# Kernel optimization log

Measured on AMD Instinct MI355X. Metric: run time of the kernel, lower is better.

Reference implementation:

```python
import jax, jax.numpy as jnp
import numpy as np

H = 768
NH = 12
DH = H // NH  # 64
EPS = 1e-6


def _split_heads(x):
    # [B,S,H] -> [B,NH,S,DH]
    B, S, _ = x.shape
    return x.reshape(B, S, NH, DH).transpose(0, 2, 1, 3)


def setup_inputs() -> dict:
    key = jax.random.key(0)
    ks = jax.random.split(key, 16)
    B, S = 4, 1024
    sc = 0.02
    return {
        "hidden_states": jax.random.normal(ks[0], (B, S, H), jnp.float32),
        "time_embeddings": jax.random.normal(ks[1], (B, S, H), jnp.float32),
        "space_embeddings": jax.random.normal(ks[2], (B, S, H), jnp.float32),
        "attention_mask": jnp.zeros((B, 1, 1, S), jnp.float32),
        "Wq": jax.random.normal(ks[3], (H, H), jnp.float32) * sc,
        "bq": jnp.zeros((H,), jnp.float32),
        "Wk": jax.random.normal(ks[4], (H, H), jnp.float32) * sc,
        "bk": jnp.zeros((H,), jnp.float32),
        "Wv": jax.random.normal(ks[5], (H, H), jnp.float32) * sc,
        "bv": jnp.zeros((H,), jnp.float32),
        "Wt": jax.random.normal(ks[6], (H, H), jnp.float32) * sc,
        "bt": jnp.zeros((H,), jnp.float32),
        "Ws": jax.random.normal(ks[7], (H, H), jnp.float32) * sc,
        "bs": jnp.zeros((H,), jnp.float32),
    }


def reference(hidden_states, time_embeddings, space_embeddings, attention_mask,
              Wq, bq, Wk, bk, Wv, bv, Wt, bt, Ws, bs):
    q = _split_heads(hidden_states @ Wq.T + bq)   # [B,NH,S,DH]
    k = _split_heads(hidden_states @ Wk.T + bk)
    v = _split_heads(hidden_states @ Wv.T + bv)
    T = _split_heads(time_embeddings @ Wt.T + bt)
    Sp = _split_heads(space_embeddings @ Ws.T + bs)

    base = jnp.einsum("bhqd,bhkd->bhqk", q, k)
    T_norm = jnp.linalg.norm(T, axis=-1, keepdims=True)          # [B,NH,S,1]
    time_sim = jnp.einsum("bhqd,bhkd->bhqk", T, T) / (T_norm + EPS)
    S_norm = jnp.linalg.norm(Sp, axis=-1, keepdims=True)
    space_sim = jnp.einsum("bhqd,bhkd->bhqk", Sp, Sp) / (S_norm + EPS)

    scores = base * time_sim * space_sim / jnp.sqrt(jnp.float32(DH))
    scores = scores + attention_mask
    probs = jax.nn.softmax(scores, axis=-1)  # dropout is identity in eval
    ctx = jnp.einsum("bhqk,bhkd->bhqd", probs, v)
    B, _, S, _ = ctx.shape
    return ctx.transpose(0, 2, 1, 3).reshape(B, S, H)
```

## Files before the change

### kernel.cpp

```cpp
#include <hip/hip_runtime.h>

#define NHEADS 12
#define SEQ    1024
#define HDIM   768
#define DHEAD  64
#define BH_TOT 48
#define EPSN   1e-6f

typedef __attribute__((ext_vector_type(8))) short    bf8;
typedef __attribute__((ext_vector_type(4))) float    fx4;
typedef __attribute__((ext_vector_type(4))) _Float16 h4;

#define SZT 3145728u
#define WSZ 589824u

__device__ __forceinline__ float bf2f(unsigned short h) {
  union { unsigned int u; float f; } v; v.u = ((unsigned int)h) << 16; return v.f;
}
__device__ __forceinline__ unsigned short f2bf(float f) {
  union { float f; unsigned int u; } v; v.f = f;
  unsigned int u = v.u;
  return (unsigned short)((u + 0x7FFFu + ((u >> 16) & 1u)) >> 16);
}

typedef __attribute__((address_space(3))) unsigned int lds_u32;
typedef __attribute__((address_space(1))) const unsigned int glb_u32;
__device__ __forceinline__ void gld16(const unsigned short* g, unsigned short* l) {
  __builtin_amdgcn_global_load_lds((glb_u32*)g, (lds_u32*)l, 16, 0, 0);
}

__global__ void convert_kernel(const float* __restrict__ hs, const float* __restrict__ te,
                               const float* __restrict__ se,
                               const float* __restrict__ Wq, const float* __restrict__ Wk,
                               const float* __restrict__ Wv, const float* __restrict__ Wt,
                               const float* __restrict__ Ws2,
                               unsigned short* __restrict__ ws)
{
  const int z = blockIdx.y;
  const float* src;
  unsigned short* dst;
  int n;
  if (z < 3) {
    src = (z == 0) ? hs : (z == 1) ? te : se;
    dst = ws + (size_t)(5 + z) * SZT;
    n = 3145728;
  } else {
    src = (z == 3) ? Wq : (z == 4) ? Wk : (z == 5) ? Wv : (z == 6) ? Wt : Ws2;
    dst = ws + (size_t)8 * SZT + (size_t)(z - 3) * WSZ;
    n = 589824;
  }
  const int base = (blockIdx.x * 256 + threadIdx.x) * 8;
  if (base >= n) return;
  const fx4 a = *(const fx4*)(src + base);
  const fx4 b = *(const fx4*)(src + base + 4);
  bf8 o;
#pragma unroll
  for (int j = 0; j < 4; ++j) { o[j] = (short)f2bf(a[j]); o[4 + j] = (short)f2bf(b[j]); }
  *(bf8*)(dst + base) = o;
}

__global__ __launch_bounds__(256, 3)
void proj_kernel(unsigned short* __restrict__ ws,
                 const float* __restrict__ bq, const float* __restrict__ bk,
                 const float* __restrict__ bv, const float* __restrict__ bt,
                 const float* __restrict__ bs)
{
  __shared__ unsigned short Xs[2][4096];
  __shared__ unsigned short Ys[2][4096];

  const int z = blockIdx.z;
  const unsigned short* X = ws + (size_t)5 * SZT + (size_t)((z < 3) ? 0 : (z - 2)) * SZT;
  const unsigned short* W = ws + (size_t)8 * SZT + (size_t)z * WSZ;
  const float* bias = (z == 0) ? bq : (z == 1) ? bk : (z == 2) ? bv : (z == 3) ? bt : bs;
  unsigned short* out = ws + (size_t)((z < 2) ? z : (z == 2) ? 4 : (z == 3) ? 2 : 3) * SZT;

  const int tid   = threadIdx.x;
  const int lane  = tid & 63;
  const int wid   = tid >> 6;
  const int wm    = wid >> 1, wn = wid & 1;
  const int colid = lane & 15, quad = lane >> 4;
  const int m0 = blockIdx.y * 128, n0 = blockIdx.x * 128;

  auto stage = [&](int kt, int pb) {
#pragma unroll
    for (int i = 0; i < 2; ++i) {
      const int slot = i * 256 + tid;
      const int row = slot >> 2, ch = slot & 3;
      gld16(X + (m0 + row) * HDIM + kt + ch * 8, &Xs[pb][slot * 8]);
      gld16(W + (n0 + row) * HDIM + kt + ch * 8, &Ys[pb][slot * 8]);
    }
  };

  fx4 acc[4][4];
#pragma unroll
  for (int i = 0; i < 4; ++i)
#pragma unroll
    for (int j = 0; j < 4; ++j) acc[i][j] = (fx4){0.f, 0.f, 0.f, 0.f};

  stage(0, 0);
  __syncthreads();

  for (int it = 0; it < 24; ++it) {
    const int pb = it & 1;
    if (it + 1 < 24) stage((it + 1) * 32, pb ^ 1);

    bf8 af[4], bfr[4];
#pragma unroll
    for (int i = 0; i < 4; ++i)
      af[i] = *(const bf8*)&Xs[pb][(wm * 64 + i * 16 + colid) * 32 + quad * 8];
#pragma unroll
    for (int j = 0; j < 4; ++j)
      bfr[j] = *(const bf8*)&Ys[pb][(wn * 64 + j * 16 + colid) * 32 + quad * 8];
#pragma unroll
    for (int i = 0; i < 4; ++i)
#pragma unroll
      for (int j = 0; j < 4; ++j)
        acc[i][j] = __builtin_amdgcn_mfma_f32_16x16x32_bf16(af[i], bfr[j], acc[i][j], 0, 0, 0);
    __syncthreads();
  }

  if (z != 2) {
#pragma unroll
    for (int i = 0; i < 4; ++i) {
      const int r0 = m0 + wm * 64 + i * 16 + quad * 4;
      const int bb = r0 >> 10, s0 = r0 & 1023;
#pragma unroll
      for (int j = 0; j < 4; ++j) {
        const int c = n0 + wn * 64 + j * 16 + colid;
        const int h = c >> 6, d = c & 63;
        const float bvl = bias[c];
        unsigned short* op = out + (((bb * NHEADS + h) * SEQ + s0) * DHEAD + d);
#pragma unroll
        for (int reg = 0; reg < 4; ++reg)
          op[reg * DHEAD] = f2bf(acc[i][j][reg] + bvl);
      }
    }
  } else {
#pragma unroll
    for (int i = 0; i < 4; ++i) {
      const int r0 = m0 + wm * 64 + i * 16 + quad * 4;
      const int bb = r0 >> 10, s0 = r0 & 1023;
#pragma unroll
      for (int j = 0; j < 4; ++j) {
        const int c = n0 + wn * 64 + j * 16 + colid;
        const int h = c >> 6, d = c & 63;
        const float bvl = bias[c];
        h4 pk;
#pragma unroll
        for (int reg = 0; reg < 4; ++reg)
          pk[reg] = (_Float16)(acc[i][j][reg] + bvl);
        *(h4*)(void*)(out + ((size_t)((bb * NHEADS + h) * DHEAD + d)) * SEQ + s0) = pk;
      }
    }
  }
}

__global__ __launch_bounds__(128, 2)
void attn_kernel(const unsigned short* __restrict__ ws,
                 const float* __restrict__ maskb,
                 float* __restrict__ outb)
{
  const unsigned short* Qb  = ws;
  const unsigned short* GT0 = ws + (size_t)1 * SZT;
  const unsigned short* GT1 = ws + (size_t)2 * SZT;
  const unsigned short* GT2 = ws + (size_t)3 * SZT;
  const _Float16* Vtf = (const _Float16*)(ws + (size_t)4 * SZT);

  __shared__ unsigned short Ls[2][3][64][64];

  const int tid   = threadIdx.x;
  const int lane  = tid & 63;
  const int wid   = tid >> 6;
  const int colid = lane & 15, quad = lane >> 4;

  const int lin = blockIdx.x;
  const int xcd = lin & 7;
  const int idx = lin >> 3;
  const int bh  = xcd * 6 + (idx % 6);
  const int qx  = idx / 6;
  const int b   = bh / NHEADS, h = bh % NHEADS;
  const int q0  = qx * 64 + wid * 32;
  const int base_h = bh * SEQ * DHEAD;

  bf8 bqf[2][2], btf[2][2], bsf[2][2];
  float rs[2];
#pragma unroll
  for (int g = 0; g < 2; ++g) {
    const int row = q0 + g * 16 + colid;
    const unsigned short* qp = Qb  + base_h + row * 64 + quad * 8;
    const unsigned short* tp = GT1 + base_h + row * 64 + quad * 8;
    const unsigned short* sp = GT2 + base_h + row * 64 + quad * 8;
    bqf[g][0] = *(const bf8*)qp;  bqf[g][1] = *(const bf8*)(qp + 32);
    btf[g][0] = *(const bf8*)tp;  btf[g][1] = *(const bf8*)(tp + 32);
    bsf[g][0] = *(const bf8*)sp;  bsf[g][1] = *(const bf8*)(sp + 32);
    float t2 = 0.f, s2 = 0.f;
#pragma unroll
    for (int fr = 0; fr < 2; ++fr)
#pragma unroll
      for (int j = 0; j < 8; ++j) {
        const float tv = bf2f((unsigned short)btf[g][fr][j]);
        const float sv2 = bf2f((unsigned short)bsf[g][fr][j]);
        t2 += tv * tv; s2 += sv2 * sv2;
      }
    t2 += __shfl_xor(t2, 16); t2 += __shfl_xor(t2, 32);
    s2 += __shfl_xor(s2, 16); s2 += __shfl_xor(s2, 32);
    rs[g] = 1.0f / ((sqrtf(t2) + EPSN) * (sqrtf(s2) + EPSN) * 8.0f);
  }

  auto stage = [&](int kb, int pb) {
#pragma unroll
    for (int i = 0; i < 12; ++i) {
      const int s  = i * 128 + tid;
      const int r  = (s >> 3) & 63;
      const int cs = ((s & 7) ^ (r & 7)) * 8;
      unsigned short* dst = &Ls[pb][0][0][0] + s * 8;
      if (i < 4)      gld16(GT0 + base_h + (kb + r) * 64 + cs, dst);
      else if (i < 8) gld16(GT1 + base_h + (kb + r) * 64 + cs, dst);
      else            gld16(GT2 + base_h + (kb + r) * 64 + cs, dst);
    }
  };

  float m_[2], l_[2];
  fx4 o[2][4];
#pragma unroll
  for (int g = 0; g < 2; ++g) {
    m_[g] = -1.0e30f; l_[g] = 0.f;
#pragma unroll
    for (int fd = 0; fd < 4; ++fd) o[g][fd] = (fx4){0.f, 0.f, 0.f, 0.f};
  }
  const fx4 zero = (fx4){0.f, 0.f, 0.f, 0.f};

  stage(0, 0);
  __syncthreads();

#pragma unroll 1
  for (int t = 0; t < 16; ++t) {
    const int pb = t & 1;
    if (t + 1 < 16) stage((t + 1) * 64, pb ^ 1);
    const int kb = t * 64;

#pragma unroll
    for (int hh = 0; hh < 2; ++hh) {
      bf8 ak[2][2], at_[2][2], as_[2][2];
      h4 vv[2][4];
      fx4 mk[2];
#pragma unroll
      for (int ff = 0; ff < 2; ++ff) {
        const int f   = hh * 2 + ff;
        const int row = f * 16 + colid;
        const int sw  = row & 7;
#pragma unroll
        for (int fr = 0; fr < 2; ++fr) {
          const int co = ((quad + fr * 4) ^ sw) * 8;
          ak[ff][fr]  = *(const bf8*)&Ls[pb][0][row][co];
          at_[ff][fr] = *(const bf8*)&Ls[pb][1][row][co];
          as_[ff][fr] = *(const bf8*)&Ls[pb][2][row][co];
        }
#pragma unroll
        for (int fd = 0; fd < 4; ++fd)
          vv[ff][fd] = *(const h4*)(Vtf + (size_t)(bh * DHEAD + fd * 16 + colid) * SEQ
                                        + kb + f * 16 + quad * 4);
        mk[ff] = *(const fx4*)(maskb + b * SEQ + kb + f * 16 + quad * 4);
      }

#pragma unroll
      for (int g = 0; g < 2; ++g) {
        float sv[2][4];
#pragma unroll
        for (int ff = 0; ff < 2; ++ff) {
          fx4 ab = __builtin_amdgcn_mfma_f32_16x16x32_bf16(ak[ff][0], bqf[g][0], zero, 0, 0, 0);
          ab = __builtin_amdgcn_mfma_f32_16x16x32_bf16(ak[ff][1], bqf[g][1], ab, 0, 0, 0);
          fx4 tt = __builtin_amdgcn_mfma_f32_16x16x32_bf16(at_[ff][0], btf[g][0], zero, 0, 0, 0);
          tt = __builtin_amdgcn_mfma_f32_16x16x32_bf16(at_[ff][1], btf[g][1], tt, 0, 0, 0);
          fx4 ss = __builtin_amdgcn_mfma_f32_16x16x32_bf16(as_[ff][0], bsf[g][0], zero, 0, 0, 0);
          ss = __builtin_amdgcn_mfma_f32_16x16x32_bf16(as_[ff][1], bsf[g][1], ss, 0, 0, 0);
#pragma unroll
          for (int reg = 0; reg < 4; ++reg)
            sv[ff][reg] = (ab[reg] * tt[reg]) * ss[reg] * rs[g] + mk[ff][reg];
        }

        float bm = sv[0][0];
#pragma unroll
        for (int ff = 0; ff < 2; ++ff)
#pragma unroll
          for (int reg = 0; reg < 4; ++reg) bm = fmaxf(bm, sv[ff][reg]);
        bm = fmaxf(bm, __shfl_xor(bm, 16));
        bm = fmaxf(bm, __shfl_xor(bm, 32));
        const float mn = fmaxf(m_[g], bm);
        const float alpha = __expf(m_[g] - mn);
        float rsum = 0.f;
        h4 pa[2];
#pragma unroll
        for (int ff = 0; ff < 2; ++ff)
#pragma unroll
          for (int reg = 0; reg < 4; ++reg) {
            const float p = __expf(sv[ff][reg] - mn);
            rsum += p;
            pa[ff][reg] = (_Float16)p;
          }
        rsum += __shfl_xor(rsum, 16);
        rsum += __shfl_xor(rsum, 32);
        l_[g] = l_[g] * alpha + rsum;
        m_[g] = mn;

        float ar[4];
#pragma unroll
        for (int reg = 0; reg < 4; ++reg) ar[reg] = __shfl(alpha, quad * 4 + reg);
#pragma unroll
        for (int fd = 0; fd < 4; ++fd)
#pragma unroll
          for (int reg = 0; reg < 4; ++reg) o[g][fd][reg] *= ar[reg];

#pragma unroll
        for (int ff = 0; ff < 2; ++ff)
#pragma unroll
          for (int fd = 0; fd < 4; ++fd)
            o[g][fd] = __builtin_amdgcn_mfma_f32_16x16x16f16(pa[ff], vv[ff][fd], o[g][fd], 0, 0, 0);
      }
    }
    __syncthreads();
  }

#pragma unroll
  for (int g = 0; g < 2; ++g) {
    const float linv = 1.0f / l_[g];
    float ir[4];
#pragma unroll
    for (int reg = 0; reg < 4; ++reg) ir[reg] = __shfl(linv, quad * 4 + reg);
#pragma unroll
    for (int reg = 0; reg < 4; ++reg) {
      const int s = q0 + g * 16 + quad * 4 + reg;
#pragma unroll
      for (int fd = 0; fd < 4; ++fd)
        outb[(size_t)(b * SEQ + s) * HDIM + h * DHEAD + fd * 16 + colid] = o[g][fd][reg] * ir[reg];
    }
  }
}

extern "C" void kernel_launch(void* const* d_in, const int* in_sizes, int n_in,
                              void* d_out, int out_size, void* d_ws, size_t ws_size,
                              hipStream_t stream)
{
  (void)in_sizes; (void)n_in; (void)out_size; (void)ws_size;
  const float* hs   = (const float*)d_in[0];
  const float* te   = (const float*)d_in[1];
  const float* se   = (const float*)d_in[2];
  const float* mask = (const float*)d_in[3];
  const float* Wq   = (const float*)d_in[4];
  const float* bq   = (const float*)d_in[5];
  const float* Wk   = (const float*)d_in[6];
  const float* bk   = (const float*)d_in[7];
  const float* Wv   = (const float*)d_in[8];
  const float* bv   = (const float*)d_in[9];
  const float* Wt   = (const float*)d_in[10];
  const float* bt   = (const float*)d_in[11];
  const float* Wsp  = (const float*)d_in[12];
  const float* bsp  = (const float*)d_in[13];
  float* out = (float*)d_out;
  unsigned short* ws = (unsigned short*)d_ws;

  convert_kernel<<<dim3(1536, 8), 256, 0, stream>>>(hs, te, se, Wq, Wk, Wv, Wt, Wsp, ws);
  proj_kernel<<<dim3(6, 32, 5), 256, 0, stream>>>(ws, bq, bk, bv, bt, bsp);
  attn_kernel<<<dim3(768), 128, 0, stream>>>(ws, mask, out);
}
```

Measured before the change: 212.7 us.

## Split attention key range across two wave pairs and merge partial softmax states

New measurement: 214.7 us. No clear change (+0.9%).

```diff
diff --git a/kernel.cpp b/kernel.cpp
--- a/kernel.cpp
+++ b/kernel.cpp
@@ -155,7 +155,7 @@
   }
 }
 
-__global__ __launch_bounds__(128, 2)
+__global__ __launch_bounds__(256, 3)
 void attn_kernel(const unsigned short* __restrict__ ws,
                  const float* __restrict__ maskb,
                  float* __restrict__ outb)
@@ -166,11 +166,13 @@
   const unsigned short* GT2 = ws + (size_t)3 * SZT;
   const _Float16* Vtf = (const _Float16*)(ws + (size_t)4 * SZT);
 
-  __shared__ unsigned short Ls[2][3][64][64];
+  __shared__ unsigned short Ls[2][2][3][32][64];
 
   const int tid   = threadIdx.x;
   const int lane  = tid & 63;
   const int wid   = tid >> 6;
+  const int wq    = wid & 1;
+  const int wp    = wid >> 1;
   const int colid = lane & 15, quad = lane >> 4;
 
   const int lin = blockIdx.x;
@@ -179,8 +181,9 @@
   const int bh  = xcd * 6 + (idx % 6);
   const int qx  = idx / 6;
   const int b   = bh / NHEADS, h = bh % NHEADS;
-  const int q0  = qx * 64 + wid * 32;
+  const int q0  = qx * 64 + wq * 32;
   const int base_h = bh * SEQ * DHEAD;
+  const int kbase  = wp * 512;
 
   bf8 bqf[2][2], btf[2][2], bsf[2][2];
   float rs[2];
@@ -200,23 +203,25 @@
       for (int j = 0; j < 8; ++j) {
         const float tv = bf2f((unsigned short)btf[g][fr][j]);
         const float sv2 = bf2f((unsigned short)bsf[g][fr][j]);
-        t2 += tv * tv; s2 += sv2 * sv2;
+        t2 += tv * tv; s2 += sv2 * s2 * 0.f + sv2 * sv2;
       }
     t2 += __shfl_xor(t2, 16); t2 += __shfl_xor(t2, 32);
     s2 += __shfl_xor(s2, 16); s2 += __shfl_xor(s2, 32);
     rs[g] = 1.0f / ((sqrtf(t2) + EPSN) * (sqrtf(s2) + EPSN) * 8.0f);
   }
 
-  auto stage = [&](int kb, int pb) {
-#pragma unroll
-    for (int i = 0; i < 12; ++i) {
-      const int s  = i * 128 + tid;
-      const int r  = (s >> 3) & 63;
-      const int cs = ((s & 7) ^ (r & 7)) * 8;
-      unsigned short* dst = &Ls[pb][0][0][0] + s * 8;
-      if (i < 4)      gld16(GT0 + base_h + (kb + r) * 64 + cs, dst);
-      else if (i < 8) gld16(GT1 + base_h + (kb + r) * 64 + cs, dst);
-      else            gld16(GT2 + base_h + (kb + r) * 64 + cs, dst);
+  auto stage = [&](int t, int pb) {
+#pragma unroll
+    for (int i = 0; i < 6; ++i) {
+      const int p  = (i >= 3) ? 1 : 0;
+      const int tz = i - p * 3;
+      const int kb = p * 512 + t * 32;
+      const int r  = tid >> 3;
+      const int cs = ((tid & 7) ^ (r & 7)) * 8;
+      unsigned short* dst = &Ls[pb][0][0][0][0] + (size_t)(i * 256 + tid) * 8;
+      const unsigned short* src =
+          ((tz == 0) ? GT0 : (tz == 1) ? GT1 : GT2) + base_h + (kb + r) * 64 + cs;
+      gld16(src, dst);
     }
   };
 
@@ -236,103 +241,130 @@
 #pragma unroll 1
   for (int t = 0; t < 16; ++t) {
     const int pb = t & 1;
-    if (t + 1 < 16) stage((t + 1) * 64, pb ^ 1);
-    const int kb = t * 64;
-
-#pragma unroll
-    for (int hh = 0; hh < 2; ++hh) {
-      bf8 ak[2][2], at_[2][2], as_[2][2];
-      h4 vv[2][4];
-      fx4 mk[2];
+    if (t + 1 < 16) stage(t + 1, pb ^ 1);
+    const int kb = kbase + t * 32;
+
+    bf8 ak[2][2], at_[2][2], as_[2][2];
+    h4 vv[2][4];
+    fx4 mk[2];
+#pragma unroll
+    for (int ff = 0; ff < 2; ++ff) {
+      const int row = ff * 16 + colid;
+      const int sw  = row & 7;
+#pragma unroll
+      for (int fr = 0; fr < 2; ++fr) {
+        const int co = ((quad + fr * 4) ^ sw) * 8;
+        ak[ff][fr]  = *(const bf8*)&Ls[pb][wp][0][row][co];
+        at_[ff][fr] = *(const bf8*)&Ls[pb][wp][1][row][co];
+        as_[ff][fr] = *(const bf8*)&Ls[pb][wp][2][row][co];
+      }
+#pragma unroll
+      for (int fd = 0; fd < 4; ++fd)
+        vv[ff][fd] = *(const h4*)(Vtf + (size_t)(bh * DHEAD + fd * 16 + colid) * SEQ
+                                      + kb + ff * 16 + quad * 4);
+      mk[ff] = *(const fx4*)(maskb + b * SEQ + kb + ff * 16 + quad * 4);
+    }
+
+#pragma unroll
+    for (int g = 0; g < 2; ++g) {
+      float sv[2][4];
 #pragma unroll
       for (int ff = 0; ff < 2; ++ff) {
-        const int f   = hh * 2 + ff;
-        const int row = f * 16 + colid;
-        const int sw  = row & 7;
-#pragma unroll
-        for (int fr = 0; fr < 2; ++fr) {
-          const int co = ((quad + fr * 4) ^ sw) * 8;
-          ak[ff][fr]  = *(const bf8*)&Ls[pb][0][row][co];
-          at_[ff][fr] = *(const bf8*)&Ls[pb][1][row][co];
-          as_[ff][fr] = *(const bf8*)&Ls[pb][2][row][co];
+        fx4 ab = __builtin_amdgcn_mfma_f32_16x16x32_bf16(ak[ff][0], bqf[g][0], zero, 0, 0, 0);
+        ab = __builtin_amdgcn_mfma_f32_16x16x32_bf16(ak[ff][1], bqf[g][1], ab, 0, 0, 0);
+        fx4 tt = __builtin_amdgcn_mfma_f32_16x16x32_bf16(at_[ff][0], btf[g][0], zero, 0, 0, 0);
+        tt = __builtin_amdgcn_mfma_f32_16x16x32_bf16(at_[ff][1], btf[g][1], tt, 0, 0, 0);
+        fx4 ss = __builtin_amdgcn_mfma_f32_16x16x32_bf16(as_[ff][0], bsf[g][0], zero, 0, 0, 0);
+        ss = __builtin_amdgcn_mfma_f32_16x16x32_bf16(as_[ff][1], bsf[g][1], ss, 0, 0, 0);
+#pragma unroll
+        for (int reg = 0; reg < 4; ++reg)
+          sv[ff][reg] = (ab[reg] * tt[reg]) * ss[reg] * rs[g] + mk[ff][reg];
+      }
+
+      float bm = sv[0][0];
+#pragma unroll
+      for (int ff = 0; ff < 2; ++ff)
+#pragma unroll
+        for (int reg = 0; reg < 4; ++reg) bm = fmaxf(bm, sv[ff][reg]);
+      bm = fmaxf(bm, __shfl_xor(bm, 16));
+      bm = fmaxf(bm, __shfl_xor(bm, 32));
+      const float mn = fmaxf(m_[g], bm);
+      const float alpha = __expf(m_[g] - mn);
+      float rsum = 0.f;
+      h4 pa[2];
+#pragma unroll
+      for (int ff = 0; ff < 2; ++ff)
+#pragma unroll
+        for (int reg = 0; reg < 4; ++reg) {
+          const float p = __expf(sv[ff][reg] - mn);
+          rsum += p;
+          pa[ff][reg] = (_Float16)p;
         }
+      rsum += __shfl_xor(rsum, 16);
+      rsum += __shfl_xor(rsum, 32);
+      l_[g] = l_[g] * alpha + rsum;
+      m_[g] = mn;
+
+      float ar[4];
+#pragma unroll
+      for (int reg = 0; reg < 4; ++reg) ar[reg] = __shfl(alpha, quad * 4 + reg);
+#pragma unroll
+      for (int fd = 0; fd < 4; ++fd)
+#pragma unroll
+        for (int reg = 0; reg < 4; ++reg) o[g][fd][reg] *= ar[reg];
+
+#pragma unroll
+      for (int ff = 0; ff < 2; ++ff)
 #pragma unroll
         for (int fd = 0; fd < 4; ++fd)
-          vv[ff][fd] = *(const h4*)(Vtf + (size_t)(bh * DHEAD + fd * 16 + colid) * SEQ
-                                        + kb + f * 16 + quad * 4);
-        mk[ff] = *(const fx4*)(maskb + b * SEQ + kb + f * 16 + quad * 4);
-      }
-
-#pragma unroll
-      for (int g = 0; g < 2; ++g) {
-        float sv[2][4];
-#pragma unroll
-        for (int ff = 0; ff < 2; ++ff) {
-          fx4 ab = __builtin_amdgcn_mfma_f32_16x16x32_bf16(ak[ff][0], bqf[g][0], zero, 0, 0, 0);
-          ab = __builtin_amdgcn_mfma_f32_16x16x32_bf16(ak[ff][1], bqf[g][1], ab, 0, 0, 0);
-          fx4 tt = __builtin_amdgcn_mfma_f32_16x16x32_bf16(at_[ff][0], btf[g][0], zero, 0, 0, 0);
-          tt = __builtin_amdgcn_mfma_f32_16x16x32_bf16(at_[ff][1], btf[g][1], tt, 0, 0, 0);
-          fx4 ss = __builtin_amdgcn_mfma_f32_16x16x32_bf16(as_[ff][0], bsf[g][0], zero, 0, 0, 0);
-          ss = __builtin_amdgcn_mfma_f32_16x16x32_bf16(as_[ff][1], bsf[g][1], ss, 0, 0, 0);
-#pragma unroll
-          for (int reg = 0; reg < 4; ++reg)
-            sv[ff][reg] = (ab[reg] * tt[reg]) * ss[reg] * rs[g] + mk[ff][reg];
+          o[g][fd] = __builtin_amdgcn_mfma_f32_16x16x16f16(pa[ff], vv[ff][fd], o[g][fd], 0, 0, 0);
+    }
+    __syncthreads();
+  }
+
+  float* Lsf = (float*)&Ls[0][0][0][0][0];
+  if (wid >= 2) {
+    const int w2 = wid - 2;
+#pragma unroll
+    for (int g = 0; g < 2; ++g) {
+#pragma unroll
+      for (int fd = 0; fd < 4; ++fd)
+#pragma unroll
+        for (int reg = 0; reg < 4; ++reg)
+          Lsf[((((w2 * 2 + g) * 4 + fd) * 4 + reg) * 64) + lane] = o[g][fd][reg];
+      if (quad == 0) {
+        Lsf[4096 + (w2 * 2 + g) * 16 + colid] = m_[g];
+        Lsf[4096 + 64 + (w2 * 2 + g) * 16 + colid] = l_[g];
+      }
+    }
+  }
+  __syncthreads();
+  if (wid < 2) {
+    const int w2 = wid;
+#pragma unroll
+    for (int g = 0; g < 2; ++g) {
+      const float m1v = Lsf[4096 + (w2 * 2 + g) * 16 + colid];
+      const float l1v = Lsf[4096 + 64 + (w2 * 2 + g) * 16 + colid];
+      const float M   = fmaxf(m_[g], m1v);
+      const float a0  = __expf(m_[g] - M), a1 = __expf(m1v - M);
+      const float li  = 1.0f / (l_[g] * a0 + l1v * a1);
+      const float c0 = a0 * li, c1 = a1 * li;
+      float s0[4], s1[4];
+#pragma unroll
+      for (int reg = 0; reg < 4; ++reg) {
+        s0[reg] = __shfl(c0, quad * 4 + reg);
+        s1[reg] = __shfl(c1, quad * 4 + reg);
+      }
+#pragma unroll
+      for (int reg = 0; reg < 4; ++reg) {
+        const int s = q0 + g * 16 + quad * 4 + reg;
+#pragma unroll
+        for (int fd = 0; fd < 4; ++fd) {
+          const float val = o[g][fd][reg] * s0[reg]
+                          + Lsf[((((w2 * 2 + g) * 4 + fd) * 4 + reg) * 64) + lane] * s1[reg];
+          outb[(size_t)(b * SEQ + s) * HDIM + h * DHEAD + fd * 16 + colid] = val;
         }
-
-        float bm = sv[0][0];
-#pragma unroll
-        for (int ff = 0; ff < 2; ++ff)
-#pragma unroll
-          for (int reg = 0; reg < 4; ++reg) bm = fmaxf(bm, sv[ff][reg]);
-        bm = fmaxf(bm, __shfl_xor(bm, 16));
-        bm = fmaxf(bm, __shfl_xor(bm, 32));
-        const float mn = fmaxf(m_[g], bm);
-        const float alpha = __expf(m_[g] - mn);
-        float rsum = 0.f;
-        h4 pa[2];
-#pragma unroll
-        for (int ff = 0; ff < 2; ++ff)
-#pragma unroll
-          for (int reg = 0; reg < 4; ++reg) {
-            const float p = __expf(sv[ff][reg] - mn);
-            rsum += p;
-            pa[ff][reg] = (_Float16)p;
-          }
-        rsum += __shfl_xor(rsum, 16);
-        rsum += __shfl_xor(rsum, 32);
-        l_[g] = l_[g] * alpha + rsum;
-        m_[g] = mn;
-
-        float ar[4];
-#pragma unroll
-        for (int reg = 0; reg < 4; ++reg) ar[reg] = __shfl(alpha, quad * 4 + reg);
-#pragma unroll
-        for (int fd = 0; fd < 4; ++fd)
-#pragma unroll
-          for (int reg = 0; reg < 4; ++reg) o[g][fd][reg] *= ar[reg];
-
-#pragma unroll
-        for (int ff = 0; ff < 2; ++ff)
-#pragma unroll
-          for (int fd = 0; fd < 4; ++fd)
-            o[g][fd] = __builtin_amdgcn_mfma_f32_16x16x16f16(pa[ff], vv[ff][fd], o[g][fd], 0, 0, 0);
-      }
-    }
-    __syncthreads();
-  }
-
-#pragma unroll
-  for (int g = 0; g < 2; ++g) {
-    const float linv = 1.0f / l_[g];
-    float ir[4];
-#pragma unroll
-    for (int reg = 0; reg < 4; ++reg) ir[reg] = __shfl(linv, quad * 4 + reg);
-#pragma unroll
-    for (int reg = 0; reg < 4; ++reg) {
-      const int s = q0 + g * 16 + quad * 4 + reg;
-#pragma unroll
-      for (int fd = 0; fd < 4; ++fd)
-        outb[(size_t)(b * SEQ + s) * HDIM + h * DHEAD + fd * 16 + colid] = o[g][fd][reg] * ir[reg];
+      }
     }
   }
 }
@@ -361,5 +393,5 @@
 
   convert_kernel<<<dim3(1536, 8), 256, 0, stream>>>(hs, te, se, Wq, Wk, Wv, Wt, Wsp, ws);
   proj_kernel<<<dim3(6, 32, 5), 256, 0, stream>>>(ws, bq, bk, bv, bt, bsp);
-  attn_kernel<<<dim3(768), 128, 0, stream>>>(ws, mask, out);
-}
+  attn_kernel<<<dim3(768), 256, 0, stream>>>(ws, mask, out);
+}
```
